# Kernel optimization log

Hardware: AMD Instinct MI355X
Metric: run time of the kernel (lower is better)

Reference implementation:

```python
import jax, jax.numpy as jnp
import numpy as np

B, S, D, H, E, K, DH = 4, 1024, 1024, 8, 4, 2, 128


def setup_inputs() -> dict:
    key = jax.random.key(0)
    ks = jax.random.split(key, 9)
    std = 1.0 / np.sqrt(D)
    f = lambda k, shape, s: jax.random.normal(k, shape, dtype=jnp.float32) * s
    return {
        'q_src': f(ks[0], (B, S, D), 1.0),
        'k_src': f(ks[1], (B, S, D), 1.0),
        'v_src': f(ks[2], (B, S, D), 1.0),
        'Wq': f(ks[3], (H * DH, D), std),
        'Wk': f(ks[4], (H * DH, D), std),
        'Wv': f(ks[5], (H * E, D, DH), std),
        'Wo': f(ks[6], (H * E, DH, D), 1.0 / np.sqrt(H * DH)),
        'sel_v': f(ks[7], (H * E, D), std),
        'sel_o': f(ks[8], (H * E, D), std),
    }


def _route(src, selw):
    # sigmoid-gated per-head top-k expert selection (get_sel), eval mode
    g = jax.nn.sigmoid((src @ selw.T).reshape(*src.shape[:-1], H, E))  # [B,S,H,E]
    val, idx = jax.lax.top_k(g, K)
    # dense per-expert mixture weights: zeros except top-k sigmoid gates
    return (jax.nn.one_hot(idx, E, dtype=g.dtype) * val[..., None]).sum(-2)  # [B,S,H,E]


def reference(q_src, k_src, v_src, Wq, Wk, Wv, Wo, sel_v, sel_o):
    scale = (1.0 / np.sqrt(DH)) ** 0.5  # scale.sqrt() applied to both q and k
    q = ((q_src @ Wq.T) * scale).reshape(B, S, H, DH).transpose(0, 2, 1, 3)  # [B,H,S,DH]
    k = ((k_src @ Wk.T) * scale).reshape(B, S, H, DH).transpose(0, 2, 1, 3)

    wv = _route(k_src, sel_v)  # [B,S,H,E] V-expert gates (from keys)
    wo = _route(q_src, sel_o)  # [B,S,H,E] O-expert gates (from queries)

    # cvmm V: per-token top-k mixture of expert V projections
    v_all = jnp.einsum('bsd,hedc->bshec', v_src, Wv.reshape(H, E, D, DH))
    v = jnp.einsum('bshec,bshe->bhsc', v_all, wv)  # [B,H,S,DH]

    att = jax.nn.softmax(jnp.einsum('bhqc,bhkc->bhqk', q, k), axis=-1)
    res = jnp.einsum('bhqk,bhkc->bqhc', att, v)  # [B,S,H,DH]

    # cvmm O: weight per-head outputs by gates, project and sum over heads/experts
    resw = res[..., None, :] * wo[..., None]  # [B,S,H,E,DH]
    out = jnp.einsum('bshec,hecd->bsd', resw, Wo.reshape(H, E, DH, D))
    return out
```

## Files before the change

### kernel.cpp

```cpp
#include <hip/hip_runtime.h>

#define DEV __device__ __forceinline__

typedef __attribute__((ext_vector_type(8))) short s8v;
typedef __attribute__((ext_vector_type(4))) short s4v;
typedef __attribute__((ext_vector_type(4))) float f4v;

DEV unsigned short f2b(float f){
    unsigned u = __float_as_uint(f);
    u = (u + 0x7FFFu + ((u >> 16) & 1u)) >> 16;
    return (unsigned short)u;
}
DEV float b2f(short s){ return __uint_as_float(((unsigned)(unsigned short)s) << 16); }

DEV void gload16(const void* g, void* l){
    __builtin_amdgcn_global_load_lds(
        (const __attribute__((address_space(1))) unsigned*)g,
        (__attribute__((address_space(3))) unsigned*)l, 16, 0, 0);
}


DEV void stage2(const short* A, const short* B, int sA, int sB, int kA, int kB,
                short* la, short* lb, int w, int lane){
    int srow = lane >> 3;
    int swcol = ((lane & 7) ^ srow) << 3;
    #pragma unroll
    for(int it = 0; it < 4; it++){
        int seg = (w << 2) + it;
        int row = (seg << 3) + srow;
        gload16(&A[(size_t)row * sA + kA + swcol], &la[seg << 9]);
        gload16(&B[(size_t)row * sB + kB + swcol], &lb[seg << 9]);
    }
}

DEV void mfma_block(const short* la, const short* lb, int wm, int wn, int qr, int grp, f4v acc[4][4]){
    #pragma unroll
    for(int ks = 0; ks < 2; ks++){
        s8v af[4], bf[4];
        #pragma unroll
        for(int m = 0; m < 4; m++)
            af[m] = *(const s8v*)&la[(wm + m * 16 + qr) * 64 + ((((ks << 2) + grp) ^ (qr & 7)) << 3)];
        #pragma unroll
        for(int n = 0; n < 4; n++)
            bf[n] = *(const s8v*)&lb[(wn + n * 16 + qr) * 64 + ((((ks << 2) + grp) ^ (qr & 7)) << 3)];
        #pragma unroll
        for(int m = 0; m < 4; m++)
            #pragma unroll
            for(int n = 0; n < 4; n++)
                acc[m][n] = __builtin_amdgcn_mfma_f32_16x16x32_bf16(af[m], bf[n], acc[m][n], 0, 0, 0);
    }
}

__global__ __launch_bounds__(256) void k_cvt(const float* s0, const float* s1, const float* s2,
                                             const float* s3, const float* s4,
                                             short* o0, short* o1, short* o2, short* o3, short* o4){
    int y = blockIdx.y;
    const float* s = (y == 0) ? s0 : (y == 1) ? s1 : (y == 2) ? s2 : (y == 3) ? s3 : s4;
    short* o = (y == 0) ? o0 : (y == 1) ? o1 : (y == 2) ? o2 : (y == 3) ? o3 : o4;
    int n8 = (y < 3) ? 524288 : 131072;
    int idx = blockIdx.x * 256 + threadIdx.x;
    if(idx < n8){
        const float4* f = (const float4*)(s + (size_t)idx * 8);
        float4 a = f[0], b = f[1];
        s8v v;
        v[0] = f2b(a.x); v[1] = f2b(a.y); v[2] = f2b(a.z); v[3] = f2b(a.w);
        v[4] = f2b(b.x); v[5] = f2b(b.y); v[6] = f2b(b.z); v[7] = f2b(b.w);
        *(s8v*)(o + (size_t)idx * 8) = v;
    }
}

__global__ __launch_bounds__(256) void k_transpose(const float* in, short* out, int R, int C){
    in  += (size_t)blockIdx.z * R * C;
    out += (size_t)blockIdx.z * R * C;
    __shared__ float t[32][33];
    int c0 = blockIdx.x * 32, r0 = blockIdx.y * 32;
    int tx = threadIdx.x & 31, ty = threadIdx.x >> 5;
    #pragma unroll
    for(int p = 0; p < 4; p++){
        int r = p * 8 + ty;
        t[r][tx] = in[(size_t)(r0 + r) * C + c0 + tx];
    }
    __syncthreads();
    #pragma unroll
    for(int p = 0; p < 4; p++){
        int c = p * 8 + ty;
        out[(size_t)(c0 + c) * R + r0 + tx] = (short)f2b(t[tx][c]);
    }
}

__global__ __launch_bounds__(256) void k_route(const float* qsrc, const float* ksrc,
                                               const float* selv, const float* selo,
                                               float* wvp, float* wop){
    int which = blockIdx.y;
    const float* src = which ? qsrc : ksrc;
    const float* sel = which ? selo : selv;
    float* wout = which ? wop : wvp;
    int w = threadIdx.x >> 6, lane = threadIdx.x & 63;
    int token = blockIdx.x * 4 + w;
    const float4* srow = (const float4*)(src + (size_t)token * 1024 + lane * 16);
    float x[16];
    #pragma unroll
    for(int q = 0; q < 4; q++){
        float4 v = srow[q];
        x[q*4+0] = v.x; x[q*4+1] = v.y; x[q*4+2] = v.z; x[q*4+3] = v.w;
    }
    __shared__ float gs[4][32];
    for(int e = 0; e < 32; e++){
        const float4* sr = (const float4*)(sel + (size_t)e * 1024 + lane * 16);
        float acc = 0.f;
        #pragma unroll
        for(int q = 0; q < 4; q++){
            float4 v = sr[q];
            acc = fmaf(x[q*4+0], v.x, acc);
            acc = fmaf(x[q*4+1], v.y, acc);
            acc = fmaf(x[q*4+2], v.z, acc);
            acc = fmaf(x[q*4+3], v.w, acc);
        }
        #pragma unroll
        for(int off = 1; off < 64; off <<= 1) acc += __shfl_xor(acc, off);
        if(lane == 0) gs[w][e] = 1.0f / (1.0f + expf(-acc));
    }
    if(lane < 8){
        float g[4];
        #pragma unroll
        for(int e = 0; e < 4; e++) g[e] = gs[w][lane * 4 + e];
        #pragma unroll
        for(int e = 0; e < 4; e++){
            int rank = 0;
            #pragma unroll
            for(int j = 0; j < 4; j++)
                rank += (g[j] > g[e]) || (g[j] == g[e] && j < e);
            wout[(size_t)token * 32 + lane * 4 + e] = (rank < 2) ? g[e] : 0.0f;
        }
    }
}

__global__ __launch_bounds__(256) void k_gemmqk(const short* qsb, const short* ksb,
                                                const short* wqb, const short* wkb,
                                                short* qo, short* ko, float scale){
    __shared__ __align__(16) short la[2][8192];
    __shared__ __align__(16) short lb[2][8192];
    int wg = (blockIdx.x & 7) * 64 + (blockIdx.x >> 3);
    int which = wg >> 8, tl = wg & 255;
    int mt = tl >> 3, nt = tl & 7;
    const short* A = (which ? ksb : qsb) + ((size_t)(mt << 7)) * 1024;
    const short* B = (which ? wkb : wqb) + ((size_t)(nt << 7)) * 1024;
    short* out = which ? ko : qo;
    int tid = threadIdx.x, lane = tid & 63, w = tid >> 6;
    int wm = (w >> 1) << 6, wn = (w & 1) << 6;
    int qr = lane & 15, grp = lane >> 4;
    f4v acc[4][4];
    #pragma unroll
    for(int m = 0; m < 4; m++)
        #pragma unroll
        for(int n = 0; n < 4; n++) acc[m][n] = f4v{0.f, 0.f, 0.f, 0.f};
    #pragma unroll 1
    for(int t = -1; t < 16; t++){
        int nxt = t + 1;
        if(nxt < 16)
            stage2(A, B, 1024, 1024, nxt << 6, nxt << 6, la[nxt & 1], lb[nxt & 1], w, lane);
        if(t >= 0)
            mfma_block(la[t & 1], lb[t & 1], wm, wn, qr, grp, acc);
        __syncthreads();
    }
    #pragma unroll
    for(int m = 0; m < 4; m++){
        int rb = (mt << 7) + wm + m * 16 + (grp << 2);
        #pragma unroll
        for(int n = 0; n < 4; n++){
            int col = (nt << 7) + wn + n * 16 + qr;
            #pragma unroll
            for(int r = 0; r < 4; r++)
                out[(size_t)(rb + r) * 1024 + col] = (short)f2b(acc[m][n][r] * scale);
        }
    }
}

__global__ __launch_bounds__(256) void k_gemmva(const short* A, const short* B, short* C){
    __shared__ __align__(16) short la[8192];
    __shared__ __align__(16) short lb[8192];
    int wg = (blockIdx.x & 7) * 128 + (blockIdx.x >> 3);
    int mt = wg >> 5, nt = wg & 31;
    int i0 = mt << 7, j0 = nt << 7;
    const short* Ab = A + (size_t)i0 * 1024;
    const short* Bb = B + (size_t)j0 * 1024;
    int tid = threadIdx.x, lane = tid & 63, w = tid >> 6;
    int wm = (w >> 1) << 6, wn = (w & 1) << 6;
    int qr = lane & 15, grp = lane >> 4;
    f4v acc[4][4];
    #pragma unroll
    for(int m = 0; m < 4; m++)
        #pragma unroll
        for(int n = 0; n < 4; n++) acc[m][n] = f4v{0.f, 0.f, 0.f, 0.f};
    #pragma unroll 1
    for(int t = 0; t < 16; t++){
        stage2(Ab, Bb, 1024, 1024, t << 6, t << 6, la, lb, w, lane);
        __syncthreads();
        mfma_block(la, lb, wm, wn, qr, grp, acc);
        __syncthreads();
    }
    #pragma unroll
    for(int m = 0; m < 4; m++){
        int rb = i0 + wm + m * 16 + (grp << 2);
        #pragma unroll
        for(int n = 0; n < 4; n++){
            int col = j0 + wn + n * 16 + qr;
            #pragma unroll
            for(int r = 0; r < 4; r++)
                C[(size_t)(rb + r) * 4096 + col] = (short)f2b(acc[m][n][r]);
        }
    }
}

__global__ __launch_bounds__(256) void k_vredg(const short* vall, const float* wv, short* vtg){
    int bh = blockIdx.y, b = bh >> 3, h = bh & 7;
    int s0 = blockIdx.x * 32;
    constexpr int LDT = 520;
    __shared__ __align__(16) short tile[32 * LDT];
    __shared__ float gsm[32][4];
    int tid = threadIdx.x;
    #pragma unroll
    for(int p = 0; p < 8; p++){
        int chunk = tid + p * 256;
        int row = chunk >> 6, cc = (chunk & 63) << 3;
        int token = b * 1024 + s0 + row;
        *(s8v*)&tile[row * LDT + cc] = *(const s8v*)&vall[(size_t)token * 4096 + h * 512 + cc];
    }
    if(tid < 128){
        int row = tid >> 2, e = tid & 3;
        gsm[row][e] = wv[(size_t)(b * 1024 + s0 + row) * 32 + h * 4 + e];
    }
    __syncthreads();
    #pragma unroll
    for(int p = 0; p < 16; p++){
        int idx = tid + p * 256;
        int s = idx & 31, c = idx >> 5;
        float v = 0.f;
        #pragma unroll
        for(int e = 0; e < 4; e++) v += b2f(tile[s * LDT + e * 128 + c]) * gsm[s][e];
        vtg[((size_t)bh * 128 + c) * 1024 + s0 + s] = (short)f2b(v);
    }
}

__global__ __launch_bounds__(256) void k_gemmo(const short* resw, const short* wot, float* po){
    __shared__ __align__(16) short la[2][8192];
    __shared__ __align__(16) short lb[2][8192];
    int wg = (blockIdx.x & 7) * 64 + (blockIdx.x >> 3);
    int ksp = wg & 1, tile = wg >> 1;
    int mt = tile >> 3, nt = tile & 7;
    const short* A = resw + (size_t)(mt << 7) * 4096 + ksp * 2048;
    const short* B = wot + (size_t)(nt << 7) * 4096 + ksp * 2048;
    int tid = threadIdx.x, lane = tid & 63, w = tid >> 6;
    int wm = (w >> 1) << 6, wn = (w & 1) << 6;
    int qr = lane & 15, grp = lane >> 4;
    f4v acc[4][4];
    #pragma unroll
    for(int m = 0; m < 4; m++)
        #pragma unroll
        for(int n = 0; n < 4; n++) acc[m][n] = f4v{0.f, 0.f, 0.f, 0.f};
    #pragma unroll 1
    for(int t = -1; t < 32; t++){
        int nxt = t + 1;
        if(nxt < 32)
            stage2(A, B, 4096, 4096, nxt << 6, nxt << 6, la[nxt & 1], lb[nxt & 1], w, lane);
        if(t >= 0)
            mfma_block(la[t & 1], lb[t & 1], wm, wn, qr, grp, acc);
        __syncthreads();
    }
    po += (size_t)ksp * 4194304;
    #pragma unroll
    for(int m = 0; m < 4; m++){
        int rb = (mt << 7) + wm + m * 16 + (grp << 2);
        #pragma unroll
        for(int n = 0; n < 4; n++){
            int col = (nt << 7) + wn + n * 16 + qr;
            #pragma unroll
            for(int r = 0; r < 4; r++)
                po[(size_t)(rb + r) * 1024 + col] = acc[m][n][r];
        }
    }
}

__global__ __launch_bounds__(256) void k_red(const float* p0, const float* p1, float* out){
    size_t idx = ((size_t)blockIdx.x * 256 + threadIdx.x) * 4;
    f4v a = *(const f4v*)&p0[idx];
    f4v b = *(const f4v*)&p1[idx];
    f4v s = a + b;
    *(f4v*)&out[idx] = s;
}

__global__ __launch_bounds__(256) void k_attn(const short* qg, const short* kg,
                                              const short* vtg, short* res){
    __shared__ __align__(16) short lk[2][8192];
    __shared__ __align__(16) short lv[2][8192];
    __shared__ __align__(16) short pl[4][16 * 72];
    int bh = blockIdx.y, b = bh >> 3, h = bh & 7;
    int w = threadIdx.x >> 6, lane = threadIdx.x & 63;
    int qr = lane & 15, grp = lane >> 4;
    int q0 = blockIdx.x * 64 + w * 16;
    const short* vtb = vtg + ((size_t)bh << 17);
    short* pw = &pl[w][0];

    int tok = b * 1024 + q0 + qr;
    s8v qf[4];
    #pragma unroll
    for(int ks = 0; ks < 4; ks++)
        qf[ks] = *(const s8v*)&qg[(size_t)tok * 1024 + h * 128 + ks * 32 + grp * 8];
    f4v o[8];
    #pragma unroll
    for(int ct = 0; ct < 8; ct++) o[ct] = f4v{0.f, 0.f, 0.f, 0.f};
    float m_cur = -1e30f, l_cur = 0.f;

    int klr = lane >> 4, klc = lane & 15;
    int vlr = lane >> 3, vlc = lane & 7;

    #pragma unroll 1
    for(int t = -1; t < 16; t++){
        int nxt = t + 1;
        if(nxt < 16){
            int buf = nxt & 1, kv0 = nxt << 6;
            #pragma unroll
            for(int i = 0; i < 4; i++){
                int seg = (w << 2) + i;
                int kr = (seg << 2) + klr;
                int kc = klc ^ (kr & 7);
                gload16(&kg[(size_t)(b * 1024 + kv0 + kr) * 1024 + h * 128 + kc * 8], &lk[buf][seg << 9]);
                int vr = (seg << 3) + vlr;
                int vc = vlc ^ (vr & 7);
                gload16(&vtb[(size_t)vr * 1024 + kv0 + vc * 8], &lv[buf][seg << 9]);
            }
        }
        if(t >= 0){
            int cur = t & 1;
            f4v s[4];
            #pragma unroll
            for(int kt = 0; kt < 4; kt++) s[kt] = f4v{0.f, 0.f, 0.f, 0.f};
            __builtin_amdgcn_s_setprio(1);
            #pragma unroll
            for(int ks = 0; ks < 4; ks++){
                #pragma unroll
                for(int kt = 0; kt < 4; kt++){
                    int row = kt * 16 + qr;
                    s8v kf = *(const s8v*)&lk[cur][row * 128 + ((((ks << 2) + grp) ^ (row & 7)) << 3)];
                    s[kt] = __builtin_amdgcn_mfma_f32_16x16x32_bf16(kf, qf[ks], s[kt], 0, 0, 0);
                }
            }
            __builtin_amdgcn_s_setprio(0);
            float pm = s[0][0];
            #pragma unroll
            for(int kt = 0; kt < 4; kt++)
                #pragma unroll
                for(int r = 0; r < 4; r++) pm = fmaxf(pm, s[kt][r]);
            pm = fmaxf(pm, __shfl_xor(pm, 16));
            pm = fmaxf(pm, __shfl_xor(pm, 32));
            float mn = fmaxf(m_cur, pm);
            float fs = __expf(m_cur - mn);
            float ps = 0.f;
            #pragma unroll
            for(int kt = 0; kt < 4; kt++)
                #pragma unroll
                for(int r = 0; r < 4; r++){
                    s[kt][r] = __expf(s[kt][r] - mn);
                    ps += s[kt][r];
                }
            ps += __shfl_xor(ps, 16);
            ps += __shfl_xor(ps, 32);
            l_cur = l_cur * fs + ps;
            m_cur = mn;
            #pragma unroll
            for(int ct = 0; ct < 8; ct++){
                o[ct][0] *= fs; o[ct][1] *= fs; o[ct][2] *= fs; o[ct][3] *= fs;
            }
            #pragma unroll
            for(int kt = 0; kt < 4; kt++){
                s4v pvv;
                #pragma unroll
                for(int r = 0; r < 4; r++) pvv[r] = (short)f2b(s[kt][r]);
                *(s4v*)&pw[qr * 72 + kt * 16 + grp * 4] = pvv;
            }
            s8v pf0 = *(const s8v*)&pw[qr * 72 + grp * 8];
            s8v pf1 = *(const s8v*)&pw[qr * 72 + 32 + grp * 8];
            __builtin_amdgcn_s_setprio(1);
            #pragma unroll
            for(int ct = 0; ct < 8; ct++){
                int row = ct * 16 + qr;
                s8v vf0 = *(const s8v*)&lv[cur][row * 64 + ((grp ^ (row & 7)) << 3)];
                s8v vf1 = *(const s8v*)&lv[cur][row * 64 + (((4 + grp) ^ (row & 7)) << 3)];
                o[ct] = __builtin_amdgcn_mfma_f32_16x16x32_bf16(vf0, pf0, o[ct], 0, 0, 0);
                o[ct] = __builtin_amdgcn_mfma_f32_16x16x32_bf16(vf1, pf1, o[ct], 0, 0, 0);
            }
            __builtin_amdgcn_s_setprio(0);
        }
        __syncthreads();
    }
    float inv = 1.0f / l_cur;
    #pragma unroll
    for(int ct = 0; ct < 8; ct++){
        s4v sv;
        #pragma unroll
        for(int r = 0; r < 4; r++) sv[r] = (short)f2b(o[ct][r] * inv);
        *(s4v*)&res[(size_t)tok * 1024 + h * 128 + ct * 16 + grp * 4] = sv;
    }
}

__global__ __launch_bounds__(256) void k_expand(const short* res, const float* wo, short* resw){
    int idx = blockIdx.x * 256 + threadIdx.x;
    int t = idx >> 9;
    int u = idx & 511;
    int he = u >> 4, ci = u & 15;
    int h = he >> 2;
    float g = wo[(size_t)t * 32 + he];
    s8v r = *(const s8v*)&res[(size_t)t * 1024 + h * 128 + ci * 8];
    s8v v;
    #pragma unroll
    for(int j = 0; j < 8; j++) v[j] = (short)f2b(b2f(r[j]) * g);
    *(s8v*)&resw[(size_t)t * 4096 + u * 8] = v;
}

extern "C" void kernel_launch(void* const* d_in, const int* in_sizes, int n_in,
                              void* d_out, int out_size, void* d_ws, size_t ws_size,
                              hipStream_t stream){
    const float* q_src = (const float*)d_in[0];
    const float* k_src = (const float*)d_in[1];
    const float* v_src = (const float*)d_in[2];
    const float* Wq    = (const float*)d_in[3];
    const float* Wk    = (const float*)d_in[4];
    const float* Wv    = (const float*)d_in[5];
    const float* Wo    = (const float*)d_in[6];
    const float* selv  = (const float*)d_in[7];
    const float* selo  = (const float*)d_in[8];

    const size_t MB = 1ull << 20;
    char* ws = (char*)d_ws;
    short* qsb  = (short*)(ws + 0 * MB);
    short* ksb  = (short*)(ws + 8 * MB);
    short* vsb  = (short*)(ws + 16 * MB);
    short* wqb  = (short*)(ws + 24 * MB);
    short* wkb  = (short*)(ws + 26 * MB);
    short* wvt  = (short*)(ws + 28 * MB);
    short* wot  = (short*)(ws + 36 * MB);
    short* q    = (short*)(ws + 44 * MB);
    short* k    = (short*)(ws + 52 * MB);
    short* vt   = (short*)(ws + 60 * MB);
    short* res  = (short*)(ws + 68 * MB);
    float* wv   = (float*)(ws + 76 * MB);
    float* wo   = (float*)(ws + 76 * MB + 524288);
    short* vall = (short*)(ws + 80 * MB);
    float* po   = (float*)(ws + 80 * MB);
    short* resw = (short*)(ws + 0 * MB);

    const float qk_scale = 0.29730177875068026f;

    k_cvt<<<dim3(2048, 5), 256, 0, stream>>>(q_src, k_src, v_src, Wq, Wk, qsb, ksb, vsb, wqb, wkb);
    k_transpose<<<dim3(4, 32, 32), 256, 0, stream>>>(Wv, wvt, 1024, 128);
    k_transpose<<<dim3(32, 128, 1), 256, 0, stream>>>(Wo, wot, 4096, 1024);
    k_route<<<dim3(1024, 2), 256, 0, stream>>>(q_src, k_src, selv, selo, wv, wo);
    k_gemmqk<<<dim3(512), 256, 0, stream>>>(qsb, ksb, wqb, wkb, q, k, qk_scale);
    k_gemmva<<<dim3(1024), 256, 0, stream>>>(vsb, wvt, vall);
    k_vredg<<<dim3(32, 32), 256, 0, stream>>>(vall, wv, vt);
    k_attn<<<dim3(16, 32), 256, 0, stream>>>(q, k, vt, res);
    k_expand<<<dim3(8192), 256, 0, stream>>>(res, wo, resw);
    k_gemmo<<<dim3(512), 256, 0, stream>>>(resw, wot, po);
    k_red<<<dim3(4096), 256, 0, stream>>>(po, po + 4194304, (float*)d_out);
}
```

Before: 264.8 us.

## Tile routing logits as LDS-blocked split-K GEMM with separate finalize kernel

The per-token routing kernel, which had each wavefront do 32 dot products with a full shuffle reduction per expert, is replaced by a tiled GEMM. It stages 128 tokens by 32 K-columns of the source and the gate weights in swizzled LDS, with each thread computing a 4x4 register tile. K is split 8 ways into partial sums, and a small second kernel sums them, applies the sigmoid and does the top-2 selection. This removes the shuffle-reduction overhead and the redundant reloads of the selector weights, at the cost of an extra launch and a partial-sum buffer that is placed in reused workspace.

```diff
diff --git a/kernel.cpp b/kernel.cpp
--- a/kernel.cpp
+++ b/kernel.cpp
@@ -88,51 +88,97 @@
     }
 }
 
-__global__ __launch_bounds__(256) void k_route(const float* qsrc, const float* ksrc,
-                                               const float* selv, const float* selo,
-                                               float* wvp, float* wop){
+__global__ __launch_bounds__(256) void k_rlogits(const float* qsrc, const float* ksrc,
+                                                 const float* selv, const float* selo,
+                                                 float* part){
     int which = blockIdx.y;
     const float* src = which ? qsrc : ksrc;
     const float* sel = which ? selo : selv;
+    int tt = blockIdx.x >> 3, ks = blockIdx.x & 7;
+    int tok0 = tt << 7;
+    __shared__ float lsrc[128][36];
+    __shared__ float lsel[32][36];
+    int tid = threadIdx.x;
+    int ts = tid & 31, es = tid >> 5;
+    float acc[4][4];
+    #pragma unroll
+    for(int j = 0; j < 4; j++)
+        #pragma unroll
+        for(int i = 0; i < 4; i++) acc[j][i] = 0.f;
+
+    #pragma unroll 1
+    for(int c = 0; c < 4; c++){
+        int k0 = (ks << 7) + (c << 5);
+        {
+            int row = tid >> 1, half = tid & 1;
+            const float4* g = (const float4*)(src + (size_t)(tok0 + row) * 1024 + k0 + half * 16);
+            #pragma unroll
+            for(int qq = 0; qq < 4; qq++){
+                int qw = half * 4 + qq;
+                *(float4*)&lsrc[row][((qw + row) & 7) * 4] = g[qq];
+            }
+        }
+        {
+            int row = tid >> 3, qw = tid & 7;
+            *(float4*)&lsel[row][((qw + row) & 7) * 4] =
+                *(const float4*)(sel + (size_t)row * 1024 + k0 + qw * 4);
+        }
+        __syncthreads();
+        #pragma unroll
+        for(int q = 0; q < 8; q++){
+            float4 sv[4];
+            #pragma unroll
+            for(int i = 0; i < 4; i++){
+                int e = es * 4 + i;
+                sv[i] = *(const float4*)&lsel[e][((q + e) & 7) * 4];
+            }
+            int slot = ((q + ts) & 7) * 4;
+            #pragma unroll
+            for(int j = 0; j < 4; j++){
+                float4 xv = *(const float4*)&lsrc[ts + 32 * j][slot];
+                #pragma unroll
+                for(int i = 0; i < 4; i++){
+                    acc[j][i] = fmaf(xv.x, sv[i].x, acc[j][i]);
+                    acc[j][i] = fmaf(xv.y, sv[i].y, acc[j][i]);
+                    acc[j][i] = fmaf(xv.z, sv[i].z, acc[j][i]);
+                    acc[j][i] = fmaf(xv.w, sv[i].w, acc[j][i]);
+                }
+            }
+        }
+        __syncthreads();
+    }
+    #pragma unroll
+    for(int j = 0; j < 4; j++){
+        int token = tok0 + ts + 32 * j;
+        f4v st;
+        #pragma unroll
+        for(int i = 0; i < 4; i++) st[i] = acc[j][i];
+        *(f4v*)&part[(((size_t)(ks * 2 + which) * 4096) + token) * 32 + es * 4] = st;
+    }
+}
+
+__global__ __launch_bounds__(256) void k_rfinal(const float* part, float* wvp, float* wop){
+    int which = blockIdx.y;
     float* wout = which ? wop : wvp;
-    int w = threadIdx.x >> 6, lane = threadIdx.x & 63;
-    int token = blockIdx.x * 4 + w;
-    const float4* srow = (const float4*)(src + (size_t)token * 1024 + lane * 16);
-    float x[16];
-    #pragma unroll
-    for(int q = 0; q < 4; q++){
-        float4 v = srow[q];
-        x[q*4+0] = v.x; x[q*4+1] = v.y; x[q*4+2] = v.z; x[q*4+3] = v.w;
-    }
-    __shared__ float gs[4][32];
-    for(int e = 0; e < 32; e++){
-        const float4* sr = (const float4*)(sel + (size_t)e * 1024 + lane * 16);
-        float acc = 0.f;
-        #pragma unroll
-        for(int q = 0; q < 4; q++){
-            float4 v = sr[q];
-            acc = fmaf(x[q*4+0], v.x, acc);
-            acc = fmaf(x[q*4+1], v.y, acc);
-            acc = fmaf(x[q*4+2], v.z, acc);
-            acc = fmaf(x[q*4+3], v.w, acc);
-        }
-        #pragma unroll
-        for(int off = 1; off < 64; off <<= 1) acc += __shfl_xor(acc, off);
-        if(lane == 0) gs[w][e] = 1.0f / (1.0f + expf(-acc));
-    }
-    if(lane < 8){
-        float g[4];
-        #pragma unroll
-        for(int e = 0; e < 4; e++) g[e] = gs[w][lane * 4 + e];
-        #pragma unroll
-        for(int e = 0; e < 4; e++){
-            int rank = 0;
-            #pragma unroll
-            for(int j = 0; j < 4; j++)
-                rank += (g[j] > g[e]) || (g[j] == g[e] && j < e);
-            wout[(size_t)token * 32 + lane * 4 + e] = (rank < 2) ? g[e] : 0.0f;
-        }
-    }
+    int tid = threadIdx.x;
+    int tok = blockIdx.x * 32 + (tid >> 3), h = tid & 7;
+    f4v sum = {0.f, 0.f, 0.f, 0.f};
+    #pragma unroll
+    for(int s = 0; s < 8; s++)
+        sum += *(const f4v*)&part[(((size_t)(s * 2 + which) * 4096) + tok) * 32 + h * 4];
+    float g[4];
+    #pragma unroll
+    for(int e = 0; e < 4; e++) g[e] = 1.0f / (1.0f + expf(-sum[e]));
+    f4v out;
+    #pragma unroll
+    for(int e = 0; e < 4; e++){
+        int rank = 0;
+        #pragma unroll
+        for(int j = 0; j < 4; j++)
+            rank += (g[j] > g[e]) || (g[j] == g[e] && j < e);
+        out[e] = (rank < 2) ? g[e] : 0.0f;
+    }
+    *(f4v*)&wout[(size_t)tok * 32 + h * 4] = out;
 }
 
 __global__ __launch_bounds__(256) void k_gemmqk(const short* qsb, const short* ksb,
@@ -445,6 +491,7 @@
     short* res  = (short*)(ws + 68 * MB);
     float* wv   = (float*)(ws + 76 * MB);
     float* wo   = (float*)(ws + 76 * MB + 524288);
+    float* part = (float*)(ws + 80 * MB);
     short* vall = (short*)(ws + 80 * MB);
     float* po   = (float*)(ws + 80 * MB);
     short* resw = (short*)(ws + 0 * MB);
@@ -454,7 +501,8 @@
     k_cvt<<<dim3(2048, 5), 256, 0, stream>>>(q_src, k_src, v_src, Wq, Wk, qsb, ksb, vsb, wqb, wkb);
     k_transpose<<<dim3(4, 32, 32), 256, 0, stream>>>(Wv, wvt, 1024, 128);
     k_transpose<<<dim3(32, 128, 1), 256, 0, stream>>>(Wo, wot, 4096, 1024);
-    k_route<<<dim3(1024, 2), 256, 0, stream>>>(q_src, k_src, selv, selo, wv, wo);
+    k_rlogits<<<dim3(256, 2), 256, 0, stream>>>(q_src, k_src, selv, selo, part);
+    k_rfinal<<<dim3(128, 2), 256, 0, stream>>>(part, wv, wo);
     k_gemmqk<<<dim3(512), 256, 0, stream>>>(qsb, ksb, wqb, wkb, q, k, qk_scale);
     k_gemmva<<<dim3(1024), 256, 0, stream>>>(vsb, wvt, vall);
     k_vredg<<<dim3(32, 32), 256, 0, stream>>>(vall, wv, vt);
```

New measurement: 221.5 us. 16.4% less time.
